# Kernel optimization log

Hardware: AMD Instinct MI355X
Metric: run time of the kernel (lower is better)

## Reference

```python
import jax, jax.numpy as jnp
import numpy as np
from jax import lax

E = 4        # n_subnets
CAP = 48     # padded per-subnet batch (subnet_bs)
NB = 4       # subnet_num_block (ResBlocks per subnet)
F = 32       # num_feature
RES_SCALE = 0.1


def _conv(x, w, b):
    # x: [B,C,H,W], w: [O,I,3,3] -> SAME conv, NCHW
    y = lax.conv_general_dilated(x, w, (1, 1), 'SAME',
                                 dimension_numbers=('NCHW', 'OIHW', 'NCHW'))
    return y + b[None, :, None, None]


def _pixel_shuffle(x, r):
    B, C, H, W = x.shape
    c = C // (r * r)
    x = x.reshape(B, c, r, r, H, W)
    x = x.transpose(0, 1, 4, 2, 5, 3)          # [B,c,H,r,W,r]
    return x.reshape(B, c, H * r, W * r)


def _subnet(x, hw, hb, r1w, r1b, r2w, r2b, ew, eb, u1w, u1b, u2w, u2b, tw, tb):
    # x: [CAP,3,32,32] -> [CAP,3,128,128]
    h = _conv(x, hw, hb)                        # head
    res = h
    for i in range(NB):                         # ResBlocks: x + s*conv(relu(conv(x)))
        t = jax.nn.relu(_conv(res, r1w[i], r1b[i]))
        res = res + RES_SCALE * _conv(t, r2w[i], r2b[i])
    res = _conv(res, ew, eb) + h                # body_end + skip
    u = _pixel_shuffle(_conv(res, u1w, u1b), 2) # upscale x2
    u = _pixel_shuffle(_conv(u, u2w, u2b), 2)   # upscale x2
    return _conv(u, tw, tb)                     # tail


def setup_inputs() -> dict:
    key = jax.random.key(0)
    ks = jax.random.split(key, 24)

    def w(k, shape, fan_in):
        return jax.random.normal(k, shape, jnp.float32) * (1.0 / np.sqrt(fan_in))

    d = {}
    d['inputs'] = jax.random.normal(ks[0], (128, 3, 32, 32), jnp.float32)
    # classifier: conv3->32 + relu + GAP + linear 32->E
    d['cls_w'] = w(ks[1], (32, 3, 3, 3), 27)
    d['cls_b'] = jnp.zeros((32,), jnp.float32)
    d['cls_fw'] = w(ks[2], (E, 32), 32)
    d['cls_fb'] = jnp.zeros((E,), jnp.float32)
    # stacked per-expert subnet params (leading dim E)
    d['head_w'] = w(ks[3], (E, F, 3, 3, 3), 27)
    d['head_b'] = jnp.zeros((E, F), jnp.float32)
    d['rb_w1'] = w(ks[4], (E, NB, F, F, 3, 3), F * 9)
    d['rb_b1'] = jnp.zeros((E, NB, F), jnp.float32)
    d['rb_w2'] = w(ks[5], (E, NB, F, F, 3, 3), F * 9)
    d['rb_b2'] = jnp.zeros((E, NB, F), jnp.float32)
    d['end_w'] = w(ks[6], (E, F, F, 3, 3), F * 9)
    d['end_b'] = jnp.zeros((E, F), jnp.float32)
    d['up_w1'] = w(ks[7], (E, 4 * F, F, 3, 3), F * 9)
    d['up_b1'] = jnp.zeros((E, 4 * F), jnp.float32)
    d['up_w2'] = w(ks[8], (E, 4 * F, F, 3, 3), F * 9)
    d['up_b2'] = jnp.zeros((E, 4 * F), jnp.float32)
    d['tail_w'] = w(ks[9], (E, 3, F, 3, 3), F * 9)
    d['tail_b'] = jnp.zeros((E, 3), jnp.float32)
    return d


def reference(inputs, cls_w, cls_b, cls_fw, cls_fb, head_w, head_b,
              rb_w1, rb_b1, rb_w2, rb_b2, end_w, end_b,
              up_w1, up_b1, up_w2, up_b2, tail_w, tail_b):
    N = inputs.shape[0]
    # classifier scores -> hard routing (argmax)
    c = jax.nn.relu(_conv(inputs, cls_w, cls_b)).mean((2, 3))   # [N,32]
    scores = c @ cls_fw.T + cls_fb                              # [N,E]
    assign = jnp.argmax(scores, axis=-1)                        # [N]

    # scatter: per-expert sorted position lists, padded to CAP (sentinel N)
    pos = jnp.where(assign[None, :] == jnp.arange(E)[:, None],
                    jnp.arange(N)[None, :], N)                  # [E,N]
    pos = jnp.sort(pos, axis=1)[:, :CAP]                        # [E,CAP]
    valid = pos < N
    safe = jnp.minimum(pos, N - 1)
    x_all = inputs[safe] * valid[:, :, None, None, None]        # [E,CAP,3,32,32]

    # horizontally-fused experts via vmap over expert dim
    y_all = jax.vmap(_subnet)(x_all, head_w, head_b, rb_w1, rb_b1, rb_w2, rb_b2,
                              end_w, end_b, up_w1, up_b1, up_w2, up_b2,
                              tail_w, tail_b)                   # [E,CAP,3,128,128]

    # gather: place real rows back at their original batch positions
    y_all = y_all * valid[:, :, None, None, None]
    out = jnp.zeros((N, 3, 128, 128), y_all.dtype)
    out = out.at[safe.reshape(-1)].add(y_all.reshape(-1, 3, 128, 128))
    return out
```

## Files before the change

### kernel.cpp

```cpp
#include <hip/hip_runtime.h>

#define EXPN 4
#define CAP 48
#define NSLOT 192
#define NBLK 4

#define OFF_RB1 0
#define OFF_RB2 36864
#define OFF_END 73728
#define OFF_UP1 82944
#define OFF_UP2 119808
#define OFF_TAIL 156672
#define PER_E 157536

typedef __attribute__((ext_vector_type(8))) short bf16x8;
typedef __attribute__((ext_vector_type(4))) float f32x4;

static __device__ __forceinline__ float bf2f(unsigned short s) {
  union { unsigned u; float f; } c; c.u = ((unsigned)s) << 16; return c.f;
}
static __device__ __forceinline__ unsigned short f2bf(float f) {
  union { float f; unsigned u; } c; c.f = f;
  unsigned u = c.u;
  return (unsigned short)((u + 0x7fffu + ((u >> 16) & 1u)) >> 16);
}
static __device__ __forceinline__ f32x4 mfma16(bf16x8 a, bf16x8 b, f32x4 c) {
  return __builtin_amdgcn_mfma_f32_16x16x32_bf16(a, b, c, 0, 0, 0);
}
static __device__ __forceinline__ float relu_f(float x) { return fmaxf(x, 0.f); }

__global__ void k_zero(float4* __restrict__ p, int n4) {
  int i = blockIdx.x * blockDim.x + threadIdx.x;
  int stride = gridDim.x * blockDim.x;
  for (; i < n4; i += stride) p[i] = make_float4(0.f, 0.f, 0.f, 0.f);
}

__global__ __launch_bounds__(256) void k_wxform(
    const float* __restrict__ rb_w1, const float* __restrict__ rb_w2,
    const float* __restrict__ end_w, const float* __restrict__ up_w1,
    const float* __restrict__ up_w2, const float* __restrict__ tail_w,
    unsigned short* __restrict__ wt) {
  int idx = blockIdx.x * 256 + threadIdx.x;
  if (idx >= EXPN * PER_E) return;
  int e = idx / PER_E, r = idx % PER_E;
  const float* src;
  int c, OC;
  if (r < OFF_RB2) {
    int i = r / 9216; c = r % 9216; OC = 32;
    src = rb_w1 + ((size_t)e * NBLK + i) * 9216;
  } else if (r < OFF_END) {
    int i = (r - OFF_RB2) / 9216; c = (r - OFF_RB2) % 9216; OC = 32;
    src = rb_w2 + ((size_t)e * NBLK + i) * 9216;
  } else if (r < OFF_UP1) {
    c = r - OFF_END; OC = 32;
    src = end_w + (size_t)e * 9216;
  } else if (r < OFF_UP2) {
    c = r - OFF_UP1; OC = 128;
    src = up_w1 + (size_t)e * 36864;
  } else if (r < OFF_TAIL) {
    c = r - OFF_UP2; OC = 128;
    src = up_w2 + (size_t)e * 36864;
  } else {
    c = r - OFF_TAIL; OC = 3;
    src = tail_w + (size_t)e * 864;
  }
  int tap = c / (OC * 32);
  int rem = c % (OC * 32);
  int och = rem / 32, ich = rem % 32;
  wt[idx] = f2bf(src[(och * 32 + ich) * 9 + tap]);
}

__global__ __launch_bounds__(256) void k_cls_conv(
    const float* __restrict__ x, const float* __restrict__ cw,
    const float* __restrict__ cb, float* __restrict__ part) {
  int n = blockIdx.y, band = blockIdx.x, t = threadIdx.x;
  int og = t >> 6, r = (t >> 3) & 7, cg = t & 7;
  int c0 = cg * 4;
  __shared__ float wl[3 * 32 * 9];
  __shared__ float tile[3 * 10 * 34];
  for (int k = t; k < 864; k += 256) {
    int o = k / 27;
    int rem = k % 27;
    int ci = rem / 9, tap = rem % 9;
    wl[(ci * 32 + o) * 9 + tap] = cw[k];
  }
  const float* inb = x + (size_t)n * 3072;
  for (int k = t; k < 1020; k += 256) {
    int ci = k / 340;
    int rem = k % 340;
    int lr = rem / 34, lc = rem % 34;
    int gr = band * 8 - 1 + lr, gc = lc - 1;
    float v = 0.f;
    if (gr >= 0 && gr < 32 && gc >= 0 && gc < 32) v = inb[(ci * 32 + gr) * 32 + gc];
    tile[k] = v;
  }
  __syncthreads();
  float acc[8][4];
#pragma unroll
  for (int oi = 0; oi < 8; ++oi) {
    float b = cb[og * 8 + oi];
#pragma unroll
    for (int p = 0; p < 4; ++p) acc[oi][p] = b;
  }
#pragma unroll
  for (int ci = 0; ci < 3; ++ci) {
    float iv[3][6];
#pragma unroll
    for (int ky = 0; ky < 3; ++ky)
#pragma unroll
      for (int dx = 0; dx < 6; ++dx)
        iv[ky][dx] = tile[ci * 340 + (r + ky) * 34 + c0 + dx];
#pragma unroll
    for (int oi = 0; oi < 8; ++oi) {
      const float* w9 = &wl[((size_t)ci * 32 + og * 8 + oi) * 9];
#pragma unroll
      for (int ky = 0; ky < 3; ++ky)
#pragma unroll
        for (int kx = 0; kx < 3; ++kx) {
          float wv = w9[ky * 3 + kx];
#pragma unroll
          for (int p = 0; p < 4; ++p) acc[oi][p] += wv * iv[ky][p + kx];
        }
    }
  }
#pragma unroll
  for (int oi = 0; oi < 8; ++oi) {
    float s = relu_f(acc[oi][0]) + relu_f(acc[oi][1]) + relu_f(acc[oi][2]) + relu_f(acc[oi][3]);
#pragma unroll
    for (int off = 32; off >= 1; off >>= 1) s += __shfl_down(s, off, 64);
    if ((t & 63) == 0) part[((size_t)n * 4 + band) * 32 + og * 8 + oi] = s;
  }
}

__global__ void k_cls_score(const float* __restrict__ part, const float* __restrict__ fw,
                            const float* __restrict__ fb, int* __restrict__ assign, int N) {
  int n = blockIdx.x * blockDim.x + threadIdx.x;
  if (n >= N) return;
  float cm[32];
#pragma unroll
  for (int o = 0; o < 32; ++o) {
    float s = part[((size_t)n * 4 + 0) * 32 + o] + part[((size_t)n * 4 + 1) * 32 + o] +
              part[((size_t)n * 4 + 2) * 32 + o] + part[((size_t)n * 4 + 3) * 32 + o];
    cm[o] = s * (1.f / 1024.f);
  }
  float best = -1e30f;
  int bi = 0;
  for (int e = 0; e < EXPN; ++e) {
    float sc = fb[e];
#pragma unroll
    for (int o = 0; o < 32; ++o) sc += cm[o] * fw[e * 32 + o];
    if (sc > best) { best = sc; bi = e; }
  }
  assign[n] = bi;
}

__global__ void k_route(const int* __restrict__ assign, int* __restrict__ slot_img, int N) {
  if (threadIdx.x == 0 && blockIdx.x == 0) {
    int cnt[EXPN];
    for (int e = 0; e < EXPN; ++e) cnt[e] = 0;
    for (int k = 0; k < NSLOT; ++k) slot_img[k] = -1;
    for (int n = 0; n < N; ++n) {
      int e = assign[n];
      if (cnt[e] < CAP) { slot_img[e * CAP + cnt[e]] = n; cnt[e]++; }
    }
  }
}

__global__ __launch_bounds__(256) void k_head(
    const float* __restrict__ x, unsigned short* __restrict__ hbuf,
    const float* __restrict__ wglob, const float* __restrict__ bglob,
    const int* __restrict__ slot_img) {
  int slot = blockIdx.y;
  int img = slot_img[slot];
  if (img < 0) return;
  int e = slot / CAP;
  int band = blockIdx.x;
  int t = threadIdx.x;
  int og = t >> 6, r = (t >> 3) & 7, cg = t & 7;
  int c0 = cg * 4;
  __shared__ float wl[3 * 32 * 9];
  __shared__ float tile[3 * 10 * 34];
  __shared__ __align__(16) unsigned short ostg[256 * 32];
  const float* wsrc = wglob + (size_t)e * 32 * 27;
  for (int k = t; k < 864; k += 256) {
    int o = k / 27;
    int rem = k % 27;
    int ci = rem / 9, tap = rem % 9;
    wl[(ci * 32 + o) * 9 + tap] = wsrc[k];
  }
  const float* bsrc = bglob + (size_t)e * 32;
  const float* inb = x + (size_t)img * 3072;
  for (int k = t; k < 3 * 10 * 34; k += 256) {
    int ci = k / 340;
    int rem = k % 340;
    int lr = rem / 34, lc = rem % 34;
    int gr = band * 8 - 1 + lr, gc = lc - 1;
    float v = 0.f;
    if (gr >= 0 && gr < 32 && gc >= 0 && gc < 32) v = inb[(ci * 32 + gr) * 32 + gc];
    tile[k] = v;
  }
  __syncthreads();
  float acc[8][4];
#pragma unroll
  for (int oi = 0; oi < 8; ++oi) {
    float b = bsrc[og * 8 + oi];
#pragma unroll
    for (int p = 0; p < 4; ++p) acc[oi][p] = b;
  }
#pragma unroll
  for (int ci = 0; ci < 3; ++ci) {
    float iv[3][6];
#pragma unroll
    for (int ky = 0; ky < 3; ++ky)
#pragma unroll
      for (int dx = 0; dx < 6; ++dx)
        iv[ky][dx] = tile[ci * 340 + (r + ky) * 34 + c0 + dx];
#pragma unroll
    for (int oi = 0; oi < 8; ++oi) {
      const float* w9 = &wl[((size_t)ci * 32 + og * 8 + oi) * 9];
#pragma unroll
      for (int ky = 0; ky < 3; ++ky)
#pragma unroll
        for (int kx = 0; kx < 3; ++kx) {
          float wv = w9[ky * 3 + kx];
#pragma unroll
          for (int p = 0; p < 4; ++p) acc[oi][p] += wv * iv[ky][p + kx];
        }
    }
  }
#pragma unroll
  for (int oi = 0; oi < 8; ++oi)
#pragma unroll
    for (int p = 0; p < 4; ++p)
      ostg[(r * 32 + c0 + p) * 32 + og * 8 + oi] = f2bf(acc[oi][p]);
  __syncthreads();
  for (int u = t; u < 1024; u += 256) {
    int px = u >> 2, c8 = (u & 3) * 8;
    int4 v = *(const int4*)&ostg[px * 32 + c8];
    size_t gi = ((size_t)slot * 1024 + band * 256 + px) * 32 + c8;
    *(int4*)&hbuf[gi] = v;
  }
}

template <int EPI>
static __device__ __forceinline__ void conv32_lds8(
    const unsigned short* __restrict__ srcP, unsigned short* __restrict__ dstP,
    const unsigned short* __restrict__ hb,
    const unsigned short* __restrict__ wtc, const float* __restrict__ bsrc,
    int w, int l, int col, int s4) {
  bf16x8 Bf[9][2];
  f32x4 bias4[2];
#pragma unroll
  for (int n = 0; n < 2; ++n) {
    bias4[n] = *(const f32x4*)&bsrc[n * 16 + s4 * 4];
#pragma unroll
    for (int tap = 0; tap < 9; ++tap)
      Bf[tap][n] = *(const bf16x8*)&wtc[((tap * 32) + n * 16 + col) * 32 + s4 * 8];
  }
  int rbase = w * 4;
#pragma unroll
  for (int xh = 0; xh < 2; ++xh) {
    int x0 = xh * 16;
    bf16x8 Af[6][3];
#pragma unroll
    for (int rr = 0; rr < 6; ++rr)
#pragma unroll
      for (int kx = 0; kx < 3; ++kx)
        Af[rr][kx] = *(const bf16x8*)&srcP[(((rbase + rr) * 34) + x0 + col + kx) * 32 + s4 * 8];
    f32x4 acc[4][2];
#pragma unroll
    for (int m = 0; m < 4; ++m)
#pragma unroll
      for (int n = 0; n < 2; ++n) acc[m][n] = bias4[n];
    __builtin_amdgcn_s_setprio(1);
#pragma unroll
    for (int ky = 0; ky < 3; ++ky)
#pragma unroll
      for (int kx = 0; kx < 3; ++kx)
#pragma unroll
        for (int r = 0; r < 4; ++r)
#pragma unroll
          for (int n = 0; n < 2; ++n)
            acc[r][n] = mfma16(Bf[ky * 3 + kx][n], Af[r + ky][kx], acc[r][n]);
    __builtin_amdgcn_s_setprio(0);
#pragma unroll
    for (int r = 0; r < 4; ++r) {
      int row = rbase + r;
      int x = x0 + col;
      unsigned li = (unsigned)(((row + 1) * 34 + (x + 1)) * 32 + s4 * 4);
#pragma unroll
      for (int n = 0; n < 2; ++n) {
        float v0 = acc[r][n][0], v1 = acc[r][n][1], v2 = acc[r][n][2], v3 = acc[r][n][3];
        if (EPI == 0) {
          v0 = relu_f(v0); v1 = relu_f(v1); v2 = relu_f(v2); v3 = relu_f(v3);
        } else if (EPI == 1) {
          uint2 old = *(const uint2*)&dstP[li + n * 16];
          v0 = bf2f((unsigned short)(old.x & 0xffff)) + 0.1f * v0;
          v1 = bf2f((unsigned short)(old.x >> 16)) + 0.1f * v1;
          v2 = bf2f((unsigned short)(old.y & 0xffff)) + 0.1f * v2;
          v3 = bf2f((unsigned short)(old.y >> 16)) + 0.1f * v3;
        } else if (EPI == 2) {
          uint2 hv = *(const uint2*)&hb[((unsigned)(row * 32 + x)) * 32 + n * 16 + s4 * 4];
          v0 += bf2f((unsigned short)(hv.x & 0xffff));
          v1 += bf2f((unsigned short)(hv.x >> 16));
          v2 += bf2f((unsigned short)(hv.y & 0xffff));
          v3 += bf2f((unsigned short)(hv.y >> 16));
        }
        uint2 o;
        o.x = (unsigned)f2bf(v0) | ((unsigned)f2bf(v1) << 16);
        o.y = (unsigned)f2bf(v2) | ((unsigned)f2bf(v3) << 16);
        *(uint2*)&dstP[li + n * 16] = o;
      }
    }
  }
}

__global__ __launch_bounds__(512, 1) void k_body(
    const unsigned short* __restrict__ hbuf, unsigned short* __restrict__ u1,
    const unsigned short* __restrict__ wt,
    const float* __restrict__ rb_b1, const float* __restrict__ rb_b2,
    const float* __restrict__ end_b, const float* __restrict__ up_b1,
    const int* __restrict__ slot_img) {
  int slot = blockIdx.x;
  int img = slot_img[slot];
  if (img < 0) return;
  int e = slot / CAP;
  int t = threadIdx.x;
  int w = t >> 6, l = t & 63;
  int col = l & 15, s4 = l >> 4;

  __shared__ __align__(16) unsigned short resP[34 * 34 * 32];
  __shared__ __align__(16) unsigned short tP[34 * 34 * 32];
  __shared__ __align__(16) unsigned short scr[8 * 512];

  int4 z = make_int4(0, 0, 0, 0);
  for (int u = t; u < 4624; u += 512) {
    *(int4*)&resP[u * 8] = z;
    *(int4*)&tP[u * 8] = z;
  }
  __syncthreads();
  const unsigned short* hsl = hbuf + (size_t)slot * 32768;
  for (int u = t; u < 4096; u += 512) {
    int px = u >> 2, c8 = (u & 3) * 8;
    *(int4*)&resP[(((px >> 5) + 1) * 34 + (px & 31) + 1) * 32 + c8] =
        *(const int4*)&hsl[px * 32 + c8];
  }
  __syncthreads();

  unsigned short* wscr = &scr[w * 512];
  const unsigned short* wte = wt + (size_t)e * PER_E;

  for (int i = 0; i < NBLK; ++i) {
    conv32_lds8<0>(resP, tP, nullptr, wte + OFF_RB1 + i * 9216,
                   rb_b1 + (size_t)e * NBLK * 32 + i * 32, w, l, col, s4);
    __syncthreads();
    conv32_lds8<1>(tP, resP, nullptr, wte + OFF_RB2 + i * 9216,
                   rb_b2 + (size_t)e * NBLK * 32 + i * 32, w, l, col, s4);
    __syncthreads();
  }
  conv32_lds8<2>(resP, tP, hsl, wte + OFF_END, end_b + (size_t)e * 32, w, l, col, s4);
  __syncthreads();

  {
    int og = w >> 1, rh = w & 1;
    const unsigned short* wtc = wte + OFF_UP1;
    const float* bsrc = up_b1 + (size_t)e * 128;
    bf16x8 Bf[9][2];
    float bias[2];
#pragma unroll
    for (int n = 0; n < 2; ++n) {
      int och = og * 32 + n * 16 + col;
      bias[n] = bsrc[och];
#pragma unroll
      for (int tap = 0; tap < 9; ++tap)
        Bf[tap][n] = *(const bf16x8*)&wtc[((tap * 128) + och) * 32 + s4 * 8];
    }
    unsigned short* u1g = u1 + (size_t)slot * 64 * 64 * 32;
#pragma unroll
    for (int xh = 0; xh < 2; ++xh) {
      int x0 = xh * 16;
#pragma unroll
      for (int rg = 0; rg < 4; ++rg) {
        int rbase = rh * 16 + rg * 4;
        bf16x8 Af[6][3];
#pragma unroll
        for (int rr = 0; rr < 6; ++rr)
#pragma unroll
          for (int kx = 0; kx < 3; ++kx)
            Af[rr][kx] = *(const bf16x8*)&tP[(((rbase + rr) * 34) + x0 + col + kx) * 32 + s4 * 8];
        f32x4 acc[4][2];
#pragma unroll
        for (int m = 0; m < 4; ++m)
#pragma unroll
          for (int n = 0; n < 2; ++n) acc[m][n] = (f32x4){bias[n], bias[n], bias[n], bias[n]};
        __builtin_amdgcn_s_setprio(1);
#pragma unroll
        for (int ky = 0; ky < 3; ++ky)
#pragma unroll
          for (int kx = 0; kx < 3; ++kx)
#pragma unroll
            for (int r = 0; r < 4; ++r)
#pragma unroll
              for (int n = 0; n < 2; ++n)
                acc[r][n] = mfma16(Af[r + ky][kx], Bf[ky * 3 + kx][n], acc[r][n]);
        __builtin_amdgcn_s_setprio(0);
#pragma unroll
        for (int r = 0; r < 4; ++r) {
          int row = rbase + r;
#pragma unroll
          for (int n = 0; n < 2; ++n) {
            int och = og * 32 + n * 16 + col;
            int ryrx = och & 3, ccl = (och >> 2) & 7;
#pragma unroll
            for (int reg = 0; reg < 4; ++reg)
              wscr[(ryrx * 16 + s4 * 4 + reg) * 8 + ccl] = f2bf(acc[r][n][reg]);
          }
          int ryrx2 = l >> 4, px2 = l & 15;
          int4 yv = *(const int4*)&wscr[(ryrx2 * 16 + px2) * 8];
          int ry = ryrx2 >> 1, rx = ryrx2 & 1;
          int oy = 2 * row + ry, ox = 2 * (x0 + px2) + rx;
          *(int4*)&u1g[((size_t)oy * 64 + ox) * 32 + og * 8] = yv;
        }
      }
    }
  }
}

template <int HW>
__global__ __launch_bounds__(256) void k_up(
    const unsigned short* __restrict__ inbuf, unsigned short* __restrict__ outbuf,
    const unsigned short* __restrict__ wt, const float* __restrict__ bglob,
    const int* __restrict__ slot_img, int slot0) {
  int lslot = blockIdx.y;
  int slot = slot0 + lslot;
  int img = slot_img[slot];
  if (img < 0) return;
  int e = slot / CAP;
  int band = blockIdx.x;
  int t = threadIdx.x;
  int w = t >> 6, l = t & 63;
  int col = l & 15, s4 = l >> 4;
  constexpr int XP = HW + 2;
  __shared__ __align__(16) unsigned short tile[4 * 10 * XP * 8];
  __shared__ __align__(16) unsigned short scr[4 * 512];
  const unsigned short* inb = inbuf + (size_t)slot * 32 * HW * HW;
  for (int u = t; u < 4 * 10 * XP; u += 256) {
    int s = u / (10 * XP);
    int rem = u - s * (10 * XP);
    int lr = rem / XP, lx = rem - lr * XP;
    int gr = band * 8 - 1 + lr, gx = lx - 1;
    int4 v = make_int4(0, 0, 0, 0);
    if (gr >= 0 && gr < HW && gx >= 0 && gx < HW)
      v = *(const int4*)&inb[(gr * HW + gx) * 32 + s * 8];
    *(int4*)&tile[u * 8] = v;
  }
  const unsigned short* wtc = wt + (size_t)e * PER_E + OFF_UP2;
  const float* bsrc = bglob + (size_t)e * 128;
  bf16x8 Bf[9][2];
  float bias[2];
#pragma unroll
  for (int n = 0; n < 2; ++n) {
    int och = w * 32 + n * 16 + col;
    bias[n] = bsrc[och];
#pragma unroll
    for (int tap = 0; tap < 9; ++tap)
      Bf[tap][n] = *(const bf16x8*)&wtc[((tap * 128) + och) * 32 + s4 * 8];
  }
  __syncthreads();
  unsigned short* wscr = &scr[w * 512];
  unsigned short* outb = outbuf + (size_t)lslot * (2 * HW) * (2 * HW) * 32;
  for (int h = 0; h < HW / 16; ++h) {
#pragma unroll
    for (int rg = 0; rg < 2; ++rg) {
      int rbase = rg * 4;
      bf16x8 Af[6][3];
#pragma unroll
      for (int rr = 0; rr < 6; ++rr)
#pragma unroll
        for (int kx = 0; kx < 3; ++kx)
          Af[rr][kx] =
              *(const bf16x8*)&tile[((s4 * 10 + rbase + rr) * XP + h * 16 + kx + col) * 8];
      f32x4 acc[4][2];
#pragma unroll
      for (int m = 0; m < 4; ++m)
#pragma unroll
        for (int n = 0; n < 2; ++n) acc[m][n] = (f32x4){bias[n], bias[n], bias[n], bias[n]};
#pragma unroll
      for (int ky = 0; ky < 3; ++ky)
#pragma unroll
        for (int kx = 0; kx < 3; ++kx)
#pragma unroll
          for (int r = 0; r < 4; ++r)
#pragma unroll
            for (int n = 0; n < 2; ++n)
              acc[r][n] = mfma16(Af[r + ky][kx], Bf[ky * 3 + kx][n], acc[r][n]);
#pragma unroll
      for (int r = 0; r < 4; ++r) {
        int row = band * 8 + rbase + r;
#pragma unroll
        for (int n = 0; n < 2; ++n) {
          int och = w * 32 + n * 16 + col;
          int ryrx = och & 3, ccl = (och >> 2) & 7;
#pragma unroll
          for (int reg = 0; reg < 4; ++reg)
            wscr[(ryrx * 16 + s4 * 4 + reg) * 8 + ccl] = f2bf(acc[r][n][reg]);
        }
        int ryrx2 = l >> 4, px2 = l & 15;
        int4 yv = *(const int4*)&wscr[(ryrx2 * 16 + px2) * 8];
        int ry = ryrx2 >> 1, rx = ryrx2 & 1;
        int oy = 2 * row + ry, ox = 2 * (h * 16 + px2) + rx;
        size_t oi = ((size_t)oy * (2 * HW) + ox) * 32 + w * 8;
        *(int4*)&outb[oi] = yv;
      }
    }
  }
}

__global__ __launch_bounds__(256) void k_tail(
    const unsigned short* __restrict__ inbuf, float* __restrict__ out,
    const unsigned short* __restrict__ wt, const float* __restrict__ bglob,
    const int* __restrict__ slot_img, int slot0) {
  int lslot = blockIdx.y;
  int slot = slot0 + lslot;
  int img = slot_img[slot];
  if (img < 0) return;
  int e = slot / CAP;
  int band = blockIdx.x & 15, xh = blockIdx.x >> 4;
  int t = threadIdx.x;
  int w = t >> 6, l = t & 63;
  int col = l & 15, s4 = l >> 4;
  __shared__ __align__(16) unsigned short tile[4 * 10 * 66 * 8];
  const unsigned short* inb = inbuf + (size_t)lslot * 128 * 128 * 32;
  for (int u = t; u < 2640; u += 256) {
    int s = u / 660;
    int rem = u - s * 660;
    int lr = rem / 66, lx = rem - lr * 66;
    int gr = band * 8 - 1 + lr, gx = xh * 64 - 1 + lx;
    int4 v = make_int4(0, 0, 0, 0);
    if (gr >= 0 && gr < 128 && gx >= 0 && gx < 128)
      v = *(const int4*)&inb[(gr * 128 + gx) * 32 + s * 8];
    *(int4*)&tile[u * 8] = v;
  }
  const unsigned short* wtc = wt + (size_t)e * PER_E + OFF_TAIL;
  bf16x8 Bf[9];
  float bias = 0.f;
  if (col < 3) bias = bglob[e * 3 + col];
#pragma unroll
  for (int tap = 0; tap < 9; ++tap) {
    if (col < 3)
      Bf[tap] = *(const bf16x8*)&wtc[((tap * 3) + col) * 32 + s4 * 8];
    else {
      bf16x8 bb;
#pragma unroll
      for (int j = 0; j < 8; ++j) bb[j] = (short)0;
      Bf[tap] = bb;
    }
  }
  __syncthreads();
  int hh = w;
#pragma unroll
  for (int rg = 0; rg < 2; ++rg) {
    int rbase = rg * 4;
    bf16x8 Af[6][3];
#pragma unroll
    for (int rr = 0; rr < 6; ++rr)
#pragma unroll
      for (int kx = 0; kx < 3; ++kx)
        Af[rr][kx] = *(const bf16x8*)&tile[((s4 * 10 + rbase + rr) * 66 + hh * 16 + kx + col) * 8];
    f32x4 acc[4];
#pragma unroll
    for (int r = 0; r < 4; ++r) acc[r] = (f32x4){bias, bias, bias, bias};
#pragma unroll
    for (int ky = 0; ky < 3; ++ky)
#pragma unroll
      for (int kx = 0; kx < 3; ++kx)
#pragma unroll
        for (int r = 0; r < 4; ++r)
          acc[r] = mfma16(Af[r + ky][kx], Bf[ky * 3 + kx], acc[r]);
    if (col < 3) {
#pragma unroll
      for (int r = 0; r < 4; ++r) {
        int grow = band * 8 + rbase + r, gx0 = xh * 64 + hh * 16 + s4 * 4;
        *(float4*)&out[(((size_t)img * 3 + col) * 128 + grow) * 128 + gx0] =
            make_float4(acc[r][0], acc[r][1], acc[r][2], acc[r][3]);
      }
    }
  }
}

extern "C" void kernel_launch(void* const* d_in, const int* in_sizes, int n_in,
                              void* d_out, int out_size, void* d_ws, size_t ws_size,
                              hipStream_t stream) {
  const float* inputs = (const float*)d_in[0];
  const float* cls_w = (const float*)d_in[1];
  const float* cls_b = (const float*)d_in[2];
  const float* cls_fw = (const float*)d_in[3];
  const float* cls_fb = (const float*)d_in[4];
  const float* head_w = (const float*)d_in[5];
  const float* head_b = (const float*)d_in[6];
  const float* rb_w1 = (const float*)d_in[7];
  const float* rb_b1 = (const float*)d_in[8];
  const float* rb_w2 = (const float*)d_in[9];
  const float* rb_b2 = (const float*)d_in[10];
  const float* end_w = (const float*)d_in[11];
  const float* end_b = (const float*)d_in[12];
  const float* up_w1 = (const float*)d_in[13];
  const float* up_b1 = (const float*)d_in[14];
  const float* up_w2 = (const float*)d_in[15];
  const float* up_b2 = (const float*)d_in[16];
  const float* tail_w = (const float*)d_in[17];
  const float* tail_b = (const float*)d_in[18];
  float* out = (float*)d_out;
  char* ws = (char*)d_ws;

  int N = in_sizes[0] / 3072;

  int* assign = (int*)ws;
  int* slot_img = (int*)(ws + 512);
  float* part = (float*)(ws + 4096);
  unsigned short* wt = (unsigned short*)(ws + 131072);
  const size_t ABUF = (size_t)NSLOT * 1024 * 32 * 2;
  const size_t U1B = (size_t)NSLOT * 64 * 64 * 32 * 2;
  const size_t SLOT_U2 = (size_t)128 * 128 * 32 * 2;
  size_t o_h = 1572864;
  unsigned short* h = (unsigned short*)(ws + o_h);
  unsigned short* u1 = (unsigned short*)(ws + o_h + ABUF);
  size_t o_u2full = o_h + ABUF + U1B;

  unsigned short* u2;
  int CH;
  size_t tail_avail = (ws_size > o_u2full) ? (ws_size - o_u2full) : 0;
  int CH_tail = (int)(tail_avail / SLOT_U2);
  const int CH_alias = (int)(ABUF / SLOT_U2);
  if (CH_tail >= CH_alias) {
    u2 = (unsigned short*)(ws + o_u2full);
    CH = CH_tail < NSLOT ? CH_tail : NSLOT;
  } else {
    u2 = (unsigned short*)(ws + o_h);
    CH = CH_alias;
  }
  if (CH < 1) CH = 1;

  k_zero<<<2048, 256, 0, stream>>>((float4*)out, out_size / 4);
  k_wxform<<<(EXPN * PER_E + 255) / 256, 256, 0, stream>>>(
      rb_w1, rb_w2, end_w, up_w1, up_w2, tail_w, wt);
  k_cls_conv<<<dim3(4, N), 256, 0, stream>>>(inputs, cls_w, cls_b, part);
  k_cls_score<<<(N + 63) / 64, 64, 0, stream>>>(part, cls_fw, cls_fb, assign, N);
  k_route<<<1, 64, 0, stream>>>(assign, slot_img, N);

  k_head<<<dim3(4, NSLOT), 256, 0, stream>>>(inputs, h, head_w, head_b, slot_img);

  k_body<<<NSLOT, 512, 0, stream>>>(h, u1, wt, rb_b1, rb_b2, end_b, up_b1, slot_img);

  for (int s0 = 0; s0 < NSLOT; s0 += CH) {
    int cur = (NSLOT - s0) < CH ? (NSLOT - s0) : CH;
    k_up<64><<<dim3(8, cur), 256, 0, stream>>>(u1, u2, wt, up_b2, slot_img, s0);
    k_tail<<<dim3(32, cur), 256, 0, stream>>>(u2, out, wt, tail_b, slot_img, s0);
  }
}
```

Baseline: 199.7 us.

## Fuse second upsample conv and tail conv into one tiled kernel

Replaces the separate k_up and k_tail kernels with a single k_uptail kernel. Each block computes the pixel-shuffled 128x128x32 intermediate for its 8x64 output tile plus halo directly into shared memory, then runs the tail conv from there. This removes the round trip of the full-resolution intermediate through global memory and the chunked launch loop. In exchange it recomputes halo rows and columns of the upsample conv, raises shared memory use per block, and adds s_setprio hints around the MFMA loops.

```diff
diff --git a/kernel.cpp b/kernel.cpp
--- a/kernel.cpp
+++ b/kernel.cpp
@@ -426,162 +426,138 @@
   }
 }
 
-template <int HW>
-__global__ __launch_bounds__(256) void k_up(
-    const unsigned short* __restrict__ inbuf, unsigned short* __restrict__ outbuf,
-    const unsigned short* __restrict__ wt, const float* __restrict__ bglob,
-    const int* __restrict__ slot_img, int slot0) {
-  int lslot = blockIdx.y;
-  int slot = slot0 + lslot;
+__global__ __launch_bounds__(256) void k_uptail(
+    const unsigned short* __restrict__ u1, float* __restrict__ out,
+    const unsigned short* __restrict__ wt, const float* __restrict__ up_b2,
+    const float* __restrict__ tail_b, const int* __restrict__ slot_img) {
+  int slot = blockIdx.y;
   int img = slot_img[slot];
   if (img < 0) return;
   int e = slot / CAP;
-  int band = blockIdx.x;
+  int b = blockIdx.x & 15;
+  int xh2 = blockIdx.x >> 4;
   int t = threadIdx.x;
   int w = t >> 6, l = t & 63;
   int col = l & 15, s4 = l >> 4;
-  constexpr int XP = HW + 2;
-  __shared__ __align__(16) unsigned short tile[4 * 10 * XP * 8];
+
+  __shared__ __align__(16) unsigned short u1t[8 * 36 * 32];
+  __shared__ __align__(16) unsigned short u2t[10 * 66 * 32];
   __shared__ __align__(16) unsigned short scr[4 * 512];
-  const unsigned short* inb = inbuf + (size_t)slot * 32 * HW * HW;
-  for (int u = t; u < 4 * 10 * XP; u += 256) {
-    int s = u / (10 * XP);
-    int rem = u - s * (10 * XP);
-    int lr = rem / XP, lx = rem - lr * XP;
-    int gr = band * 8 - 1 + lr, gx = lx - 1;
+
+  const unsigned short* u1s = u1 + (size_t)slot * 64 * 64 * 32;
+  int r0 = 4 * b - 2, c0g = 32 * xh2 - 2;
+  for (int u = t; u < 8 * 36 * 4; u += 256) {
+    int rr = u / 144;
+    int rem = u - rr * 144;
+    int cc = rem >> 2, sl = rem & 3;
+    int gy = r0 + rr, gx = c0g + cc;
     int4 v = make_int4(0, 0, 0, 0);
-    if (gr >= 0 && gr < HW && gx >= 0 && gx < HW)
-      v = *(const int4*)&inb[(gr * HW + gx) * 32 + s * 8];
-    *(int4*)&tile[u * 8] = v;
-  }
+    if (gy >= 0 && gy < 64 && gx >= 0 && gx < 64)
+      v = *(const int4*)&u1s[((size_t)gy * 64 + gx) * 32 + sl * 8];
+    *(int4*)&u1t[u * 8] = v;
+  }
+
   const unsigned short* wtc = wt + (size_t)e * PER_E + OFF_UP2;
-  const float* bsrc = bglob + (size_t)e * 128;
   bf16x8 Bf[9][2];
   float bias[2];
 #pragma unroll
   for (int n = 0; n < 2; ++n) {
     int och = w * 32 + n * 16 + col;
-    bias[n] = bsrc[och];
+    bias[n] = up_b2[(size_t)e * 128 + och];
 #pragma unroll
     for (int tap = 0; tap < 9; ++tap)
       Bf[tap][n] = *(const bf16x8*)&wtc[((tap * 128) + och) * 32 + s4 * 8];
   }
-  __syncthreads();
-  unsigned short* wscr = &scr[w * 512];
-  unsigned short* outb = outbuf + (size_t)lslot * (2 * HW) * (2 * HW) * 32;
-  for (int h = 0; h < HW / 16; ++h) {
-#pragma unroll
-    for (int rg = 0; rg < 2; ++rg) {
-      int rbase = rg * 4;
-      bf16x8 Af[6][3];
-#pragma unroll
-      for (int rr = 0; rr < 6; ++rr)
-#pragma unroll
-        for (int kx = 0; kx < 3; ++kx)
-          Af[rr][kx] =
-              *(const bf16x8*)&tile[((s4 * 10 + rbase + rr) * XP + h * 16 + kx + col) * 8];
-      f32x4 acc[4][2];
-#pragma unroll
-      for (int m = 0; m < 4; ++m)
-#pragma unroll
-        for (int n = 0; n < 2; ++n) acc[m][n] = (f32x4){bias[n], bias[n], bias[n], bias[n]};
-#pragma unroll
-      for (int ky = 0; ky < 3; ++ky)
-#pragma unroll
-        for (int kx = 0; kx < 3; ++kx)
-#pragma unroll
-          for (int r = 0; r < 4; ++r)
-#pragma unroll
-            for (int n = 0; n < 2; ++n)
-              acc[r][n] = mfma16(Af[r + ky][kx], Bf[ky * 3 + kx][n], acc[r][n]);
-#pragma unroll
-      for (int r = 0; r < 4; ++r) {
-        int row = band * 8 + rbase + r;
-#pragma unroll
-        for (int n = 0; n < 2; ++n) {
-          int och = w * 32 + n * 16 + col;
-          int ryrx = och & 3, ccl = (och >> 2) & 7;
-#pragma unroll
-          for (int reg = 0; reg < 4; ++reg)
-            wscr[(ryrx * 16 + s4 * 4 + reg) * 8 + ccl] = f2bf(acc[r][n][reg]);
-        }
-        int ryrx2 = l >> 4, px2 = l & 15;
-        int4 yv = *(const int4*)&wscr[(ryrx2 * 16 + px2) * 8];
-        int ry = ryrx2 >> 1, rx = ryrx2 & 1;
-        int oy = 2 * row + ry, ox = 2 * (h * 16 + px2) + rx;
-        size_t oi = ((size_t)oy * (2 * HW) + ox) * 32 + w * 8;
-        *(int4*)&outb[oi] = yv;
-      }
-    }
-  }
-}
-
-__global__ __launch_bounds__(256) void k_tail(
-    const unsigned short* __restrict__ inbuf, float* __restrict__ out,
-    const unsigned short* __restrict__ wt, const float* __restrict__ bglob,
-    const int* __restrict__ slot_img, int slot0) {
-  int lslot = blockIdx.y;
-  int slot = slot0 + lslot;
-  int img = slot_img[slot];
-  if (img < 0) return;
-  int e = slot / CAP;
-  int band = blockIdx.x & 15, xh = blockIdx.x >> 4;
-  int t = threadIdx.x;
-  int w = t >> 6, l = t & 63;
-  int col = l & 15, s4 = l >> 4;
-  __shared__ __align__(16) unsigned short tile[4 * 10 * 66 * 8];
-  const unsigned short* inb = inbuf + (size_t)lslot * 128 * 128 * 32;
-  for (int u = t; u < 2640; u += 256) {
-    int s = u / 660;
-    int rem = u - s * 660;
-    int lr = rem / 66, lx = rem - lr * 66;
-    int gr = band * 8 - 1 + lr, gx = xh * 64 - 1 + lx;
-    int4 v = make_int4(0, 0, 0, 0);
-    if (gr >= 0 && gr < 128 && gx >= 0 && gx < 128)
-      v = *(const int4*)&inb[(gr * 128 + gx) * 32 + s * 8];
-    *(int4*)&tile[u * 8] = v;
-  }
-  const unsigned short* wtc = wt + (size_t)e * PER_E + OFF_TAIL;
-  bf16x8 Bf[9];
-  float bias = 0.f;
-  if (col < 3) bias = bglob[e * 3 + col];
+  const unsigned short* wtt = wt + (size_t)e * PER_E + OFF_TAIL;
+  bf16x8 Bt[9];
+  float biast = 0.f;
+  if (col < 3) biast = tail_b[e * 3 + col];
 #pragma unroll
   for (int tap = 0; tap < 9; ++tap) {
     if (col < 3)
-      Bf[tap] = *(const bf16x8*)&wtc[((tap * 3) + col) * 32 + s4 * 8];
+      Bt[tap] = *(const bf16x8*)&wtt[((tap * 3) + col) * 32 + s4 * 8];
     else {
       bf16x8 bb;
 #pragma unroll
       for (int j = 0; j < 8; ++j) bb[j] = (short)0;
-      Bf[tap] = bb;
-    }
-  }
-  __syncthreads();
-  int hh = w;
-#pragma unroll
-  for (int rg = 0; rg < 2; ++rg) {
-    int rbase = rg * 4;
-    bf16x8 Af[6][3];
-#pragma unroll
-    for (int rr = 0; rr < 6; ++rr)
+      Bt[tap] = bb;
+    }
+  }
+  __syncthreads();
+
+  unsigned short* wscr = &scr[w * 512];
+#pragma unroll 1
+  for (int yy = 0; yy < 6; ++yy) {
+#pragma unroll
+    for (int xg = 0; xg < 3; ++xg) {
+      bf16x8 Af[3][3];
+#pragma unroll
+      for (int ky = 0; ky < 3; ++ky)
+#pragma unroll
+        for (int kx = 0; kx < 3; ++kx)
+          Af[ky][kx] = *(const bf16x8*)&u1t[(((yy + ky) * 36) + xg * 16 + col + kx) * 32 + s4 * 8];
+      f32x4 acc[2];
+#pragma unroll
+      for (int n = 0; n < 2; ++n) acc[n] = (f32x4){bias[n], bias[n], bias[n], bias[n]};
+      __builtin_amdgcn_s_setprio(1);
+#pragma unroll
+      for (int ky = 0; ky < 3; ++ky)
+#pragma unroll
+        for (int kx = 0; kx < 3; ++kx)
+#pragma unroll
+          for (int n = 0; n < 2; ++n)
+            acc[n] = mfma16(Af[ky][kx], Bf[ky * 3 + kx][n], acc[n]);
+      __builtin_amdgcn_s_setprio(0);
+#pragma unroll
+      for (int n = 0; n < 2; ++n) {
+        int och = w * 32 + n * 16 + col;
+        int ryrx = och & 3, ccl = (och >> 2) & 7;
+#pragma unroll
+        for (int reg = 0; reg < 4; ++reg)
+          wscr[(ryrx * 16 + s4 * 4 + reg) * 8 + ccl] = f2bf(acc[n][reg]);
+      }
+      int ryrx2 = l >> 4, px2 = l & 15;
+      int4 yv = *(const int4*)&wscr[(ryrx2 * 16 + px2) * 8];
+      int ry = ryrx2 >> 1, rx = ryrx2 & 1;
+      int oyl = 2 * yy + ry - 1;
+      int oxl = 2 * (xg * 16 + px2) + rx - 1;
+      if (oyl >= 0 && oyl < 10 && oxl >= 0 && oxl < 66) {
+        int gy2 = 8 * b - 1 + oyl;
+        int gx2 = 64 * xh2 - 1 + oxl;
+        int4 sv = (gy2 >= 0 && gy2 < 128 && gx2 >= 0 && gx2 < 128) ? yv
+                                                                   : make_int4(0, 0, 0, 0);
+        *(int4*)&u2t[((oyl * 66) + oxl) * 32 + w * 8] = sv;
+      }
+    }
+  }
+  __syncthreads();
+
+#pragma unroll
+  for (int gx = 0; gx < 4; ++gx) {
+    bf16x8 At[4][3];
+#pragma unroll
+    for (int rr = 0; rr < 4; ++rr)
 #pragma unroll
       for (int kx = 0; kx < 3; ++kx)
-        Af[rr][kx] = *(const bf16x8*)&tile[((s4 * 10 + rbase + rr) * 66 + hh * 16 + kx + col) * 8];
-    f32x4 acc[4];
-#pragma unroll
-    for (int r = 0; r < 4; ++r) acc[r] = (f32x4){bias, bias, bias, bias};
+        At[rr][kx] = *(const bf16x8*)&u2t[(((w * 2 + rr) * 66) + gx * 16 + col + kx) * 32 + s4 * 8];
+    f32x4 acc[2];
+#pragma unroll
+    for (int r = 0; r < 2; ++r) acc[r] = (f32x4){biast, biast, biast, biast};
+    __builtin_amdgcn_s_setprio(1);
 #pragma unroll
     for (int ky = 0; ky < 3; ++ky)
 #pragma unroll
       for (int kx = 0; kx < 3; ++kx)
 #pragma unroll
-        for (int r = 0; r < 4; ++r)
-          acc[r] = mfma16(Af[r + ky][kx], Bf[ky * 3 + kx], acc[r]);
+        for (int r = 0; r < 2; ++r)
+          acc[r] = mfma16(At[r + ky][kx], Bt[ky * 3 + kx], acc[r]);
+    __builtin_amdgcn_s_setprio(0);
     if (col < 3) {
 #pragma unroll
-      for (int r = 0; r < 4; ++r) {
-        int grow = band * 8 + rbase + r, gx0 = xh * 64 + hh * 16 + s4 * 4;
-        *(float4*)&out[(((size_t)img * 3 + col) * 128 + grow) * 128 + gx0] =
+      for (int r = 0; r < 2; ++r) {
+        int grow = 8 * b + w * 2 + r;
+        int gcol = 64 * xh2 + gx * 16 + s4 * 4;
+        *(float4*)&out[(((size_t)img * 3 + col) * 128 + grow) * 128 + gcol] =
             make_float4(acc[r][0], acc[r][1], acc[r][2], acc[r][3]);
       }
     }
@@ -620,26 +596,9 @@
   float* part = (float*)(ws + 4096);
   unsigned short* wt = (unsigned short*)(ws + 131072);
   const size_t ABUF = (size_t)NSLOT * 1024 * 32 * 2;
-  const size_t U1B = (size_t)NSLOT * 64 * 64 * 32 * 2;
-  const size_t SLOT_U2 = (size_t)128 * 128 * 32 * 2;
   size_t o_h = 1572864;
   unsigned short* h = (unsigned short*)(ws + o_h);
   unsigned short* u1 = (unsigned short*)(ws + o_h + ABUF);
-  size_t o_u2full = o_h + ABUF + U1B;
-
-  unsigned short* u2;
-  int CH;
-  size_t tail_avail = (ws_size > o_u2full) ? (ws_size - o_u2full) : 0;
-  int CH_tail = (int)(tail_avail / SLOT_U2);
-  const int CH_alias = (int)(ABUF / SLOT_U2);
-  if (CH_tail >= CH_alias) {
-    u2 = (unsigned short*)(ws + o_u2full);
-    CH = CH_tail < NSLOT ? CH_tail : NSLOT;
-  } else {
-    u2 = (unsigned short*)(ws + o_h);
-    CH = CH_alias;
-  }
-  if (CH < 1) CH = 1;
 
   k_zero<<<2048, 256, 0, stream>>>((float4*)out, out_size / 4);
   k_wxform<<<(EXPN * PER_E + 255) / 256, 256, 0, stream>>>(
@@ -652,9 +611,5 @@
 
   k_body<<<NSLOT, 512, 0, stream>>>(h, u1, wt, rb_b1, rb_b2, end_b, up_b1, slot_img);
 
-  for (int s0 = 0; s0 < NSLOT; s0 += CH) {
-    int cur = (NSLOT - s0) < CH ? (NSLOT - s0) : CH;
-    k_up<64><<<dim3(8, cur), 256, 0, stream>>>(u1, u2, wt, up_b2, slot_img, s0);
-    k_tail<<<dim3(32, cur), 256, 0, stream>>>(u2, out, wt, tail_b, slot_img, s0);
-  }
-}
+  k_uptail<<<dim3(32, NSLOT), 256, 0, stream>>>(u1, out, wt, up_b2, tail_b, slot_img);
+}
```

Result: no change. 197.2 us (-1.2%).
